# Optimization experiments

Hardware: AMD Instinct MI355X
Metric: run time of the kernel (lower is better)

Reference implementation:

```python
import jax, jax.numpy as jnp
import numpy as np

B, V, N, S, F, H, K, STEPS = 8, 3, 400, 1200, 16, 32, 10, 12
ALPHA_FUSE = 0.8
NEG = -9e15


def setup_inputs() -> dict:
    key = jax.random.key(0)
    ks = jax.random.split(key, 16)
    g = lambda i, shape, s=0.1: jax.random.normal(ks[i], shape, jnp.float32) * s
    return {
        "feat": jax.random.normal(ks[0], (B, S, F), jnp.float32),
        "adj": jax.random.bernoulli(ks[1], 0.05, (B, V, S, S)).astype(jnp.float32),
        "dis_lab": jax.random.uniform(ks[2], (B, K), dtype=jnp.float32),
        "W_gat": g(3, (V, F, H), 0.3),
        "a_gat": g(4, (V, 2 * H, 1), 0.3),
        "qkv_W": g(5, (H, 3 * H)),
        "qkv_b": jnp.zeros((3 * H,), jnp.float32),
        "o_W": g(6, (H, H)),
        "o_b": jnp.zeros((H,), jnp.float32),
        "fus_W": g(7, (H, H)),
        "fus_b": jnp.zeros((H,), jnp.float32),
        "att1_W": g(8, (2 * H, H)),
        "att1_b": jnp.zeros((H,), jnp.float32),
        "att2_W": g(9, (H, 1)),
        "att2_b": jnp.zeros((1,), jnp.float32),
        "gru_Wih": g(10, (H, 3 * H)),
        "gru_Whh": g(11, (H, 3 * H)),
        "gru_bih": jnp.zeros((3 * H,), jnp.float32),
        "gru_bhh": jnp.zeros((3 * H,), jnp.float32),
        "out_W": g(12, (H, 1)),
        "out_b": jnp.zeros((1,), jnp.float32),
    }


def _forward(feat, adj, dis_lab, W_gat, a_gat, qkv_W, qkv_b, o_W, o_b,
             fus_W, fus_b, att1_W, att1_b, att2_W, att2_b,
             gru_Wih, gru_Whh, gru_bih, gru_bhh, out_W, out_b):
    # ---- per-view GAT (masked softmax over dense adjacency) ----
    Wh = jnp.einsum('bsf,vfh->bvsh', feat, W_gat)            # [B,V,S,H]
    a1, a2 = a_gat[:, :H, 0], a_gat[:, H:, 0]
    e = (jnp.einsum('bvsh,vh->bvs', Wh, a1)[..., :, None]
         + jnp.einsum('bvsh,vh->bvs', Wh, a2)[..., None, :])  # [B,V,S,S]
    e = jax.nn.leaky_relu(e, 0.2)
    e = jnp.where(adj > 0, e, NEG)
    att = jax.nn.softmax(e, axis=-1)
    hid = jax.nn.elu(jnp.einsum('bvst,bvth->bvsh', att, Wh))  # [B,V,S,H]
    # ---- cross-view self-attention fusion (single head) ----
    x = hid.reshape(B, V * S, H)
    q, k, v = jnp.split(x @ qkv_W + qkv_b, 3, axis=-1)
    logits = jnp.einsum('bld,bmd->blm', q, k) / jnp.sqrt(jnp.float32(H))
    sa = jnp.einsum('blm,bmd->bld', jax.nn.softmax(logits, axis=-1), v)
    sa = sa @ o_W + o_b
    hfuse = (ALPHA_FUSE * sa + (1.0 - ALPHA_FUSE) * x).reshape(B, V, S, H)
    gate = jax.nn.sigmoid(hfuse @ fus_W + fus_b)
    fusion = jnp.sum(gate * hfuse, axis=1)[:, 2 * N:, :]      # [B,N,H]
    # ---- attention over label stations ----
    label = fusion[:, :K, :]                                  # [B,K,H]
    unlabel = fusion[:, K, :]                                 # [B,H]
    cat = jnp.concatenate([label, jnp.broadcast_to(unlabel[:, None, :], label.shape)], axis=-1)
    s = jax.nn.relu(cat @ att1_W + att1_b) @ att2_W + att2_b  # [B,K,1]
    score = jax.nn.softmax(s[..., 0] * dis_lab, axis=1)
    ctx = jnp.einsum('bk,bkh->bh', score, label)
    # ---- GRU decoder (feed hidden state back as next input) ----
    def gru_cell(xt, h):
        gi = xt @ gru_Wih + gru_bih
        gh = h @ gru_Whh + gru_bhh
        ir, iz, inn = jnp.split(gi, 3, axis=-1)
        hr, hz, hn = jnp.split(gh, 3, axis=-1)
        r = jax.nn.sigmoid(ir + hr)
        z = jax.nn.sigmoid(iz + hz)
        n = jnp.tanh(inn + r * hn)
        return (1.0 - z) * n + z * h
    def step(carry, _):
        xt, h = carry
        h2 = gru_cell(xt, h)
        out = h2 @ out_W + out_b
        return (h2, h2), out[:, 0]
    _, outs = jax.lax.scan(step, (ctx, unlabel), None, length=STEPS)
    return outs.T  # [B, STEPS]


def reference(feat, adj, dis_lab, W_gat, a_gat, qkv_W, qkv_b, o_W, o_b,
              fus_W, fus_b, att1_W, att1_b, att2_W, att2_b,
              gru_Wih, gru_Whh, gru_bih, gru_bhh, out_W, out_b):
    return _forward(feat, adj, dis_lab, W_gat, a_gat, qkv_W, qkv_b, o_W, o_b,
                    fus_W, fus_b, att1_W, att1_b, att2_W, att2_b,
                    gru_Wih, gru_Whh, gru_bih, gru_bhh, out_W, out_b)
```

## Files before the change

kernel.cpp:

```cpp
#include <hip/hip_runtime.h>
#include <math.h>

#define Bb 8
#define Vv 3
#define Ss 1200
#define SgP 1280
#define Ff 16
#define Hh 32
#define Kk 10
#define STEPS 12
#define ROWS (Bb*Vv*Ss)
#define L (Vv*Ss)
#define KPAD 1280
#define NKB 160
#define MROW 40

typedef __attribute__((ext_vector_type(8))) short bf16x8;
typedef __attribute__((ext_vector_type(4))) float f32x4;
typedef __attribute__((ext_vector_type(4))) unsigned int u32x4;

__device__ __forceinline__ unsigned int pack_hi2(float x0, float x1) {
    return (__float_as_uint(x1) & 0xFFFF0000u) | (__float_as_uint(x0) >> 16);
}
__device__ __forceinline__ unsigned int pack_lo2(float x0, float x1) {
    float h0 = __uint_as_float(__float_as_uint(x0) & 0xFFFF0000u);
    float h1 = __uint_as_float(__float_as_uint(x1) & 0xFFFF0000u);
    return (__float_as_uint(x1 - h1) & 0xFFFF0000u) | (__float_as_uint(x0 - h0) >> 16);
}
__device__ __forceinline__ unsigned int spread4(unsigned int x) {
    x = (x | (x << 12)) & 0x000F000Fu;
    x = (x | (x << 6))  & 0x03030303u;
    x = (x | (x << 3))  & 0x11111111u;
    return x;
}
__device__ __forceinline__ unsigned int enc_f(float f) {
    unsigned int u = __float_as_uint(f);
    return (u >> 31) ? ~u : (u | 0x80000000u);
}
__device__ __forceinline__ float dec_f(unsigned int e) {
    return (e >> 31) ? __uint_as_float(e & 0x7FFFFFFFu) : __uint_as_float(~e);
}

__global__ __launch_bounds__(256) void adj_pack_k(const float* __restrict__ adj,
                                                  unsigned int* __restrict__ maskb,
                                                  unsigned int* __restrict__ GmaxE) {
    if (blockIdx.x == 0 && threadIdx.x < Bb * Vv) GmaxE[threadIdx.x] = 0u;
    int gw = (blockIdx.x * 256 + threadIdx.x) >> 6;
    int lane = threadIdx.x & 63;
    for (int row = gw; row < ROWS; row += 5760) {
        const float* ar = adj + (size_t)row * Ss;
        unsigned int* mrow = maskb + (size_t)row * MROW;
        float4 a[5];
#pragma unroll
        for (int c = 0; c < 5; ++c) {
            int base = c * 256 + lane * 4;
            a[c] = (base + 3 < Ss) ? *(const float4*)(ar + base)
                                   : make_float4(0.f, 0.f, 0.f, 0.f);
        }
#pragma unroll
        for (int c = 0; c < 5; ++c) {
            unsigned long long b0 = __ballot(a[c].x > 0.f);
            unsigned long long b1 = __ballot(a[c].y > 0.f);
            unsigned long long b2 = __ballot(a[c].z > 0.f);
            unsigned long long b3 = __ballot(a[c].w > 0.f);
            int nw = (c == 4) ? 6 : 8;
            if (lane < nw) {
                int sh = 8 * lane;
                unsigned int B0 = (unsigned int)(b0 >> sh) & 0xFFu;
                unsigned int B1 = (unsigned int)(b1 >> sh) & 0xFFu;
                unsigned int B2 = (unsigned int)(b2 >> sh) & 0xFFu;
                unsigned int B3 = (unsigned int)(b3 >> sh) & 0xFFu;
                mrow[c * 8 + lane] = spread4(B0) | (spread4(B1) << 1)
                                   | (spread4(B2) << 2) | (spread4(B3) << 3);
            }
        }
        if (lane < 2) mrow[38 + lane] = 0u;
    }
}

__global__ __launch_bounds__(256) void wh_wht_k(const float* __restrict__ feat,
                                                const float* __restrict__ W_gat,
                                                const float* __restrict__ a_gat,
                                                ushort* __restrict__ WhT,
                                                float* __restrict__ fvec,
                                                float* __restrict__ gvecP,
                                                unsigned int* __restrict__ GmaxE) {
    int bv = blockIdx.x / 20, t = blockIdx.x % 20;
    int b = bv / Vv, v = bv - b * Vv;
    int s0 = t * 64;
    int tid = threadIdx.x;

    __shared__ float T[64][33];
    __shared__ float Wg[16][32];
    __shared__ float gred[8];
    for (int i = tid; i < 512; i += 256) Wg[i >> 5][i & 31] = W_gat[v * 512 + i];
    __syncthreads();

    int r8 = tid >> 5, h = tid & 31;
    float a1 = a_gat[v * 64 + h];
    float a2 = a_gat[v * 64 + 32 + h];
    float myg = -3.0e38f;
#pragma unroll
    for (int pass = 0; pass < 8; ++pass) {
        int s = s0 + pass * 8 + r8;
        float acc = 0.f;
        if (s < Ss) {
            const float4* fe = (const float4*)(feat + ((size_t)b * Ss + s) * Ff);
            float4 f0 = fe[0], f1 = fe[1], f2 = fe[2], f3 = fe[3];
            acc += f0.x * Wg[0][h]  + f0.y * Wg[1][h]  + f0.z * Wg[2][h]  + f0.w * Wg[3][h];
            acc += f1.x * Wg[4][h]  + f1.y * Wg[5][h]  + f1.z * Wg[6][h]  + f1.w * Wg[7][h];
            acc += f2.x * Wg[8][h]  + f2.y * Wg[9][h]  + f2.z * Wg[10][h] + f2.w * Wg[11][h];
            acc += f3.x * Wg[12][h] + f3.y * Wg[13][h] + f3.z * Wg[14][h] + f3.w * Wg[15][h];
        }
        T[pass * 8 + r8][h] = acc;
        float pf = acc * a1, pg = acc * a2;
#pragma unroll
        for (int m = 16; m >= 1; m >>= 1) {
            pf += __shfl_xor(pf, m);
            pg += __shfl_xor(pg, m);
        }
        if (h == 0) {
            if (s < Ss) { fvec[bv * Ss + s] = pf; myg = fmaxf(myg, pg); }
            gvecP[(size_t)bv * SgP + s] = (s < Ss) ? pg : 0.f;
        }
    }
    if (h == 0) gred[r8] = myg;
    __syncthreads();
    if (tid == 0) {
        float m = gred[0];
#pragma unroll
        for (int i = 1; i < 8; ++i) m = fmaxf(m, gred[i]);
        atomicMax(&GmaxE[bv], enc_f(m));
    }

    int hh = tid >> 3, c = tid & 7;
    int kb = t * 8 + c;
    unsigned int hb[4], lb[4];
#pragma unroll
    for (int j = 0; j < 4; ++j) {
        float e0 = T[c * 8 + 2 * j][hh], e1 = T[c * 8 + 2 * j + 1][hh];
        hb[j] = pack_hi2(e0, e1);
        lb[j] = pack_lo2(e0, e1);
    }
    size_t base = (((size_t)bv * NKB + kb) * 2) * 256 + hh * 8;
    *(uint4*)(WhT + base)       = make_uint4(hb[0], hb[1], hb[2], hb[3]);
    *(uint4*)(WhT + base + 256) = make_uint4(lb[0], lb[1], lb[2], lb[3]);
}

__global__ __launch_bounds__(256, 4) void gat_mfma_k(const unsigned int* __restrict__ maskb,
                                                     const ushort* __restrict__ WhT,
                                                     const float* __restrict__ fvec,
                                                     const float* __restrict__ gvecP,
                                                     const unsigned int* __restrict__ GmaxE,
                                                     float* __restrict__ hid,
                                                     float* __restrict__ hsel) {
    int blk = blockIdx.x;
    int bv = blk / 75, tb = blk % 75;
    int wk = threadIdx.x >> 6, lane = threadIdx.x & 63;
    int rowbase = tb * 16;
    int lr = lane & 15, kg = lane >> 4;
    int b = bv / Vv, v = bv - b * Vv;

    int ar = rowbase + lr;
    const float* g_b = gvecP + (size_t)bv * SgP;
    float fr = fvec[bv * Ss + ar];
    float M = fr + dec_f(GmaxE[bv]);
    float Mr = fmaxf(M, 0.2f * M);

    const unsigned int* mrow = maskb + (size_t)(bv * Ss + ar) * MROW + wk * 10;
    unsigned int mw[10];
#pragma unroll
    for (int i = 0; i < 5; ++i) {
        uint2 t = *(const uint2*)(mrow + 2 * i);
        mw[2 * i] = t.x; mw[2 * i + 1] = t.y;
    }

    f32x4 acc0 = {0.f, 0.f, 0.f, 0.f}, acc1 = {0.f, 0.f, 0.f, 0.f};
    float psum = 0.f;
    const ushort* Wbv = WhT + ((size_t)bv * NKB) * 512;

    int kst = wk * 320;
#pragma unroll
    for (int s = 0; s < 10; ++s) {
        int t0 = kst + s * 32 + kg * 8;
        int kb = t0 >> 3;
        unsigned int mb = (mw[s] >> (kg * 8)) & 0xFFu;

        const ushort* Bp = Wbv + (size_t)kb * 512 + lr * 8;
        bf16x8 bh0 = *(const bf16x8*)(Bp);
        bf16x8 bh1 = *(const bf16x8*)(Bp + 128);
        bf16x8 bl0 = *(const bf16x8*)(Bp + 256);
        bf16x8 bl1 = *(const bf16x8*)(Bp + 384);

        float4 gA = *(const float4*)(g_b + t0);
        float4 gB = *(const float4*)(g_b + t0 + 4);
        float gv8[8] = {gA.x, gA.y, gA.z, gA.w, gB.x, gB.y, gB.z, gB.w};
        float p[8];
#pragma unroll
        for (int j = 0; j < 8; ++j) {
            float e = fr + gv8[j];
            e = fmaxf(e, 0.2f * e);
            float pe = __expf(e - Mr);
            p[j] = ((mb >> j) & 1u) ? pe : 0.f;
            psum += p[j];
        }
        unsigned int hbp[4], lbp[4];
#pragma unroll
        for (int j = 0; j < 4; ++j) {
            hbp[j] = pack_hi2(p[2 * j], p[2 * j + 1]);
            lbp[j] = pack_lo2(p[2 * j], p[2 * j + 1]);
        }
        bf16x8 ah = __builtin_bit_cast(bf16x8, (u32x4){hbp[0], hbp[1], hbp[2], hbp[3]});
        bf16x8 al = __builtin_bit_cast(bf16x8, (u32x4){lbp[0], lbp[1], lbp[2], lbp[3]});
        acc0 = __builtin_amdgcn_mfma_f32_16x16x32_bf16(ah, bh0, acc0, 0, 0, 0);
        acc0 = __builtin_amdgcn_mfma_f32_16x16x32_bf16(ah, bl0, acc0, 0, 0, 0);
        acc0 = __builtin_amdgcn_mfma_f32_16x16x32_bf16(al, bh0, acc0, 0, 0, 0);
        acc1 = __builtin_amdgcn_mfma_f32_16x16x32_bf16(ah, bh1, acc1, 0, 0, 0);
        acc1 = __builtin_amdgcn_mfma_f32_16x16x32_bf16(ah, bl1, acc1, 0, 0, 0);
        acc1 = __builtin_amdgcn_mfma_f32_16x16x32_bf16(al, bh1, acc1, 0, 0, 0);
    }

    psum += __shfl_xor(psum, 16);
    psum += __shfl_xor(psum, 32);

    __shared__ float accS[4][2][16][17];
    __shared__ float psS[4][16];
#pragma unroll
    for (int j = 0; j < 4; ++j) {
        accS[wk][0][kg * 4 + j][lr] = acc0[j];
        accS[wk][1][kg * 4 + j][lr] = acc1[j];
    }
    if (lane < 16) psS[wk][lr] = psum;
    __syncthreads();
    if (threadIdx.x < 16)
        psS[0][threadIdx.x] += psS[1][threadIdx.x] + psS[2][threadIdx.x] + psS[3][threadIdx.x];
    __syncthreads();

    bool qb = (tb == 50);
    for (int idx = threadIdx.x; idx < 512; idx += 256) {
        int r = idx >> 5, col = idx & 31, tt = col >> 4, c = col & 15;
        float a = accS[0][tt][r][c] + accS[1][tt][r][c] + accS[2][tt][r][c] + accS[3][tt][r][c];
        float rr = a / psS[0][r];
        float hv = (rr > 0.f) ? rr : expm1f(rr);
        hid[((size_t)bv * Ss + rowbase + r) * 32 + col] = hv;
        if (qb && r < 11) hsel[(((size_t)b * Vv + v) * 11 + r) * 32 + col] = hv;
    }
}

__global__ __launch_bounds__(256) void attn_q_k(const float* __restrict__ hsel,
                                                const float* __restrict__ qkv_W,
                                                const float* __restrict__ qkv_b,
                                                float* __restrict__ qt,
                                                float* __restrict__ qc) {
    int b = blockIdx.x;
    int tid = threadIdx.x;
    __shared__ float hq[33][33];
    __shared__ float W1[32][33];
    __shared__ float W2[32][33];
    __shared__ float qS[33][33];

    for (int idx = tid; idx < 33 * 32; idx += 256) {
        int q = idx >> 5, i = idx & 31;
        int si = q / 3, v = q - si * 3;
        hq[q][i] = hsel[(((size_t)b * Vv + v) * 11 + si) * 32 + i];
    }
    for (int idx = tid; idx < 1024; idx += 256) {
        int i = idx >> 5, j = idx & 31;
        W1[i][j] = qkv_W[i * 96 + j];
        W2[i][j] = qkv_W[i * 96 + 32 + j];
    }
    __syncthreads();
    for (int idx = tid; idx < 33 * 32; idx += 256) {
        int q = idx >> 5, j = idx & 31;
        float a = qkv_b[j];
#pragma unroll
        for (int i = 0; i < 32; ++i) a += hq[q][i] * W1[i][j];
        qS[q][j] = a;
    }
    __syncthreads();
    for (int idx = tid; idx < 33 * 32; idx += 256) {
        int q = idx >> 5, i = idx & 31;
        float a = 0.f;
#pragma unroll
        for (int j = 0; j < 32; ++j) a += qS[q][j] * W2[i][j];
        qt[(size_t)b * 33 * 32 + q * 32 + i] = a;
    }
    if (tid < 33) {
        float a = 0.f;
        for (int j = 0; j < 32; ++j) a += qS[tid][j] * qkv_b[32 + j];
        qc[b * 33 + tid] = a;
    }
}

#define CH 120
#define NCH 30
#define PREC 34
__global__ __launch_bounds__(256) void attn_part_k(const float* __restrict__ hid,
                                                   const float* __restrict__ qt,
                                                   const float* __restrict__ qc,
                                                   float* __restrict__ part) {
    int blk = blockIdx.x;
    int b = blk / NCH, ch = blk % NCH;
    int k0 = ch * CH;
    int tid = threadIdx.x;
    const float inv = 0.1767766952966369f;

    __shared__ float hC[CH][33];
    __shared__ float qtS[33][33];
    __shared__ float qcS[33];
    __shared__ float lS[33][124];
    __shared__ float mS[33], lsS[33];

    for (int idx = tid; idx < CH * 32; idx += 256) {
        int r = idx >> 5, i = idx & 31;
        hC[r][i] = hid[((size_t)b * L + k0 + r) * 32 + i];
    }
    for (int idx = tid; idx < 33 * 32; idx += 256) {
        int q = idx >> 5, i = idx & 31;
        qtS[q][i] = qt[(size_t)b * 33 * 32 + q * 32 + i];
    }
    if (tid < 33) qcS[tid] = qc[b * 33 + tid];
    __syncthreads();

    for (int idx = tid; idx < 33 * CH; idx += 256) {
        int q = idx / CH, m = idx - q * CH;
        float d = 0.f;
#pragma unroll
        for (int i = 0; i < 32; ++i) d += qtS[q][i] * hC[m][i];
        lS[q][m] = (d + qcS[q]) * inv;
    }
    __syncthreads();

    int q4 = tid >> 2, j4 = tid & 3;
    if (q4 < 33) {
        float m = -3.0e38f;
        for (int k = j4; k < CH; k += 4) m = fmaxf(m, lS[q4][k]);
        m = fmaxf(m, __shfl_xor(m, 1));
        m = fmaxf(m, __shfl_xor(m, 2));
        float ssum = 0.f;
        for (int k = j4; k < CH; k += 4) {
            float p = __expf(lS[q4][k] - m);
            lS[q4][k] = p;
            ssum += p;
        }
        ssum += __shfl_xor(ssum, 1);
        ssum += __shfl_xor(ssum, 2);
        if (j4 == 0) { mS[q4] = m; lsS[q4] = ssum; }
    }
    __syncthreads();

    float* po = part + ((size_t)b * NCH + ch) * (33 * PREC);
    for (int idx = tid; idx < 33 * 32; idx += 256) {
        int q = idx >> 5, hh = idx & 31;
        float a = 0.f;
        for (int k = 0; k < CH; k += 4) {
            float4 p4 = *(const float4*)&lS[q][k];
            a += p4.x * hC[k][hh] + p4.y * hC[k+1][hh] + p4.z * hC[k+2][hh] + p4.w * hC[k+3][hh];
        }
        po[q * PREC + hh] = a;
    }
    if (tid < 33) { po[tid * PREC + 32] = mS[tid]; po[tid * PREC + 33] = lsS[tid]; }
}

__global__ __launch_bounds__(256) void comb_head_k(const float* __restrict__ part,
                                                   const float* __restrict__ hsel,
                                                   const float* __restrict__ qkv_W,
                                                   const float* __restrict__ qkv_b,
                                                   const float* __restrict__ o_W,
                                                   const float* __restrict__ o_b,
                                                   const float* __restrict__ fus_W,
                                                   const float* __restrict__ fus_b,
                                                   const float* __restrict__ dis_lab,
                                                   const float* __restrict__ att1_W,
                                                   const float* __restrict__ att1_b,
                                                   const float* __restrict__ att2_W,
                                                   const float* __restrict__ att2_b,
                                                   const float* __restrict__ Wih,
                                                   const float* __restrict__ Whh,
                                                   const float* __restrict__ bih,
                                                   const float* __restrict__ bhh,
                                                   const float* __restrict__ out_W,
                                                   const float* __restrict__ out_b,
                                                   float* __restrict__ out) {
    int b = blockIdx.x;
    int tid = threadIdx.x;
    __shared__ float RS[33][NCH];
    __shared__ float LSs[33];
    __shared__ float oS[33][33];
    __shared__ float vS[33][33];
    __shared__ float hfS[33][33];
    __shared__ float hfgS[33][32];
    __shared__ float lab[11][32];
    __shared__ float a1T[32][68];
    __shared__ float WihT[3][32][36];
    __shared__ float WhhT[3][32][36];
    __shared__ float sc[12];
    __shared__ float xS[32], hS[32];

    const float* pb = part + (size_t)b * NCH * (33 * PREC);

    if (tid < 33) {
        float M = -3.0e38f;
        for (int c = 0; c < NCH; ++c) M = fmaxf(M, pb[c * 33 * PREC + tid * PREC + 32]);
        float Lt = 0.f;
        for (int c = 0; c < NCH; ++c) {
            float w = __expf(pb[c * 33 * PREC + tid * PREC + 32] - M);
            RS[tid][c] = w;
            Lt += w * pb[c * 33 * PREC + tid * PREC + 33];
        }
        LSs[tid] = Lt;
    }
    __syncthreads();

    for (int idx = tid; idx < 33 * 32; idx += 256) {
        int q = idx >> 5, hh = idx & 31;
        float a = 0.f;
        for (int c = 0; c < NCH; ++c) a += RS[q][c] * pb[c * 33 * PREC + q * PREC + hh];
        oS[q][hh] = a / LSs[q];
    }
    __syncthreads();
    for (int idx = tid; idx < 33 * 32; idx += 256) {
        int q = idx >> 5, j = idx & 31;
        float a = qkv_b[64 + j];
#pragma unroll
        for (int i = 0; i < 32; ++i) a += oS[q][i] * qkv_W[i * 96 + 64 + j];
        vS[q][j] = a;
    }
    __syncthreads();
    for (int idx = tid; idx < 33 * 32; idx += 256) {
        int q = idx >> 5, hh = idx & 31;
        int si = q / 3, v = q - si * 3;
        float o = o_b[hh];
#pragma unroll
        for (int i = 0; i < 32; ++i) o += vS[q][i] * o_W[i * 32 + hh];
        float x = hsel[(((size_t)b * Vv + v) * 11 + si) * Hh + hh];
        hfS[q][hh] = 0.8f * o + 0.2f * x;
    }
    __syncthreads();
    for (int idx = tid; idx < 33 * 32; idx += 256) {
        int q = idx >> 5, hh = idx & 31;
        float gacc = fus_b[hh];
#pragma unroll
        for (int i = 0; i < 32; ++i) gacc += hfS[q][i] * fus_W[i * 32 + hh];
        float gate = 1.f / (1.f + __expf(-gacc));
        hfgS[q][hh] = gate * hfS[q][hh];
    }
    __syncthreads();

    for (int i = tid; i < 352; i += 256) {
        int k = i >> 5, hh = i & 31;
        lab[k][hh] = hfgS[k * 3 + 0][hh] + hfgS[k * 3 + 1][hh] + hfgS[k * 3 + 2][hh];
    }
    for (int idx = tid; idx < 2048; idx += 256) {
        int i = idx >> 5, jj = idx & 31;
        a1T[jj][i] = att1_W[idx];
    }
    for (int idx = tid; idx < 3072; idx += 256) {
        int i = idx / 96, col = idx - i * 96;
        int g = col >> 5, jj = col & 31;
        WihT[g][jj][i] = Wih[idx];
        WhhT[g][jj][i] = Whh[idx];
    }
    __syncthreads();

    int j = tid & 31, half = (tid >> 5) & 1;
    if (tid < 64) {
        float a2w = att2_W[j];
        float a1b = att1_b[j];
        float a2b = att2_b[0];
#pragma unroll
        for (int kk = 0; kk < 5; ++kk) {
            int k = 2 * kk + half;
            float t1 = a1b;
#pragma unroll
            for (int c = 0; c < 8; ++c) {
                float4 lb4 = *(const float4*)&lab[k][c * 4];
                float4 w4  = *(const float4*)&a1T[j][c * 4];
                t1 += lb4.x * w4.x + lb4.y * w4.y + lb4.z * w4.z + lb4.w * w4.w;
            }
#pragma unroll
            for (int c = 0; c < 8; ++c) {
                float4 lb4 = *(const float4*)&lab[10][c * 4];
                float4 w4  = *(const float4*)&a1T[j][32 + c * 4];
                t1 += lb4.x * w4.x + lb4.y * w4.y + lb4.z * w4.z + lb4.w * w4.w;
            }
            float val = fmaxf(t1, 0.f) * a2w;
#pragma unroll
            for (int mm = 16; mm >= 1; mm >>= 1) val += __shfl_xor(val, mm);
            if (j == 0) sc[k] = (val + a2b) * dis_lab[b * Kk + k];
        }
    }
    __syncthreads();
    if (tid == 0) {
        float mx = sc[0];
        for (int k = 1; k < 10; ++k) mx = fmaxf(mx, sc[k]);
        float sm = 0.f;
        for (int k = 0; k < 10; ++k) { sc[k] = __expf(sc[k] - mx); sm += sc[k]; }
        for (int k = 0; k < 10; ++k) sc[k] /= sm;
    }
    __syncthreads();
    if (tid < 32) {
        float c = 0.f;
        for (int k = 0; k < 10; ++k) c += sc[k] * lab[k][tid];
        xS[tid] = c;
        hS[tid] = lab[10][tid];
    }
    __syncthreads();

    float b_ir = bih[j], b_iz = bih[32 + j], b_in = bih[64 + j];
    float b_hr = bhh[j], b_hz = bhh[32 + j], b_hn = bhh[64 + j];
    float ow = out_W[j], ob = out_b[0];
    int i0 = half * 16;

    for (int t = 0; t < STEPS; ++t) {
        if (tid < 64) {
            float gi_r = 0.f, gi_z = 0.f, gi_n = 0.f;
            float gh_r = 0.f, gh_z = 0.f, gh_n = 0.f;
#pragma unroll
            for (int c = 0; c < 4; ++c) {
                float4 x4 = *(const float4*)&xS[i0 + c * 4];
                float4 h4 = *(const float4*)&hS[i0 + c * 4];
                float4 wr = *(const float4*)&WihT[0][j][i0 + c * 4];
                float4 wz = *(const float4*)&WihT[1][j][i0 + c * 4];
                float4 wn = *(const float4*)&WihT[2][j][i0 + c * 4];
                float4 ur = *(const float4*)&WhhT[0][j][i0 + c * 4];
                float4 uz = *(const float4*)&WhhT[1][j][i0 + c * 4];
                float4 un = *(const float4*)&WhhT[2][j][i0 + c * 4];
                gi_r += x4.x * wr.x + x4.y * wr.y + x4.z * wr.z + x4.w * wr.w;
                gi_z += x4.x * wz.x + x4.y * wz.y + x4.z * wz.z + x4.w * wz.w;
                gi_n += x4.x * wn.x + x4.y * wn.y + x4.z * wn.z + x4.w * wn.w;
                gh_r += h4.x * ur.x + h4.y * ur.y + h4.z * ur.z + h4.w * ur.w;
                gh_z += h4.x * uz.x + h4.y * uz.y + h4.z * uz.z + h4.w * uz.w;
                gh_n += h4.x * un.x + h4.y * un.y + h4.z * un.z + h4.w * un.w;
            }
            gi_r += __shfl_xor(gi_r, 32); gi_z += __shfl_xor(gi_z, 32); gi_n += __shfl_xor(gi_n, 32);
            gh_r += __shfl_xor(gh_r, 32); gh_z += __shfl_xor(gh_z, 32); gh_n += __shfl_xor(gh_n, 32);

            float hprev = hS[j];
            float r = 1.f / (1.f + __expf(-(gi_r + b_ir + gh_r + b_hr)));
            float z = 1.f / (1.f + __expf(-(gi_z + b_iz + gh_z + b_hz)));
            float n = tanhf(gi_n + b_in + r * (gh_n + b_hn));
            float hnew = (1.f - z) * n + z * hprev;

            float outp = hnew * ow;
#pragma unroll
            for (int mm = 16; mm >= 1; mm >>= 1) outp += __shfl_xor(outp, mm);
            if (tid == 0) out[b * STEPS + t] = outp + ob;
            if (tid < 32) { xS[32 + 0] = 0.f; }
            if (tid < 32) {  }
            if (tid < 32) { sc[11] = hnew; }
            if (tid < 32) { hS[j] = hS[j]; }
            if (tid < 32) { xS[j] = xS[j]; }
            if (tid < 32) { oS[0][j] = hnew; }
        }
        __syncthreads();
        if (tid < 32) { hS[tid] = oS[0][tid]; xS[tid] = oS[0][tid]; }
        __syncthreads();
    }
}

extern "C" void kernel_launch(void* const* d_in, const int* in_sizes, int n_in,
                              void* d_out, int out_size, void* d_ws, size_t ws_size,
                              hipStream_t stream) {
    const float* feat    = (const float*)d_in[0];
    const float* adj     = (const float*)d_in[1];
    const float* dis_lab = (const float*)d_in[2];
    const float* W_gat   = (const float*)d_in[3];
    const float* a_gat   = (const float*)d_in[4];
    const float* qkv_W   = (const float*)d_in[5];
    const float* qkv_b   = (const float*)d_in[6];
    const float* o_W     = (const float*)d_in[7];
    const float* o_b     = (const float*)d_in[8];
    const float* fus_W   = (const float*)d_in[9];
    const float* fus_b   = (const float*)d_in[10];
    const float* att1_W  = (const float*)d_in[11];
    const float* att1_b  = (const float*)d_in[12];
    const float* att2_W  = (const float*)d_in[13];
    const float* att2_b  = (const float*)d_in[14];
    const float* Wih     = (const float*)d_in[15];
    const float* Whh     = (const float*)d_in[16];
    const float* bih     = (const float*)d_in[17];
    const float* bhh     = (const float*)d_in[18];
    const float* out_W   = (const float*)d_in[19];
    const float* out_b   = (const float*)d_in[20];
    float* out = (float*)d_out;

    float* ws = (float*)d_ws;
    float*  hid    = ws;
    float*  fvec   = ws + 921600;
    float*  gvecP  = ws + 950400;
    unsigned int* GmaxE = (unsigned int*)(ws + 981120);
    ushort* WhT    = (ushort*)(ws + 981152);
    float*  part   = ws + 981152;
    float*  hsel   = ws + 1964192;
    float*  qt     = ws + 1972640;
    float*  qc     = ws + 1981088;
    unsigned int* maskb = (unsigned int*)(ws + 1981376);

    adj_pack_k<<<dim3(1440), dim3(256), 0, stream>>>(adj, maskb, GmaxE);
    wh_wht_k<<<dim3(Bb * Vv * 20), dim3(256), 0, stream>>>(feat, W_gat, a_gat,
                                                           WhT, fvec, gvecP, GmaxE);
    gat_mfma_k<<<dim3(Bb * Vv * 75), dim3(256), 0, stream>>>(maskb, WhT,
                                                             fvec, gvecP, GmaxE, hid, hsel);
    attn_q_k<<<dim3(Bb), dim3(256), 0, stream>>>(hsel, qkv_W, qkv_b, qt, qc);
    attn_part_k<<<dim3(Bb * NCH), dim3(256), 0, stream>>>(hid, qt, qc, part);
    comb_head_k<<<dim3(Bb), dim3(256), 0, stream>>>(part, hsel, qkv_W, qkv_b,
                                                    o_W, o_b, fus_W, fus_b,
                                                    dis_lab, att1_W, att1_b, att2_W, att2_b,
                                                    Wih, Whh, bih, bhh, out_W, out_b, out);
}
```

Measured before the change: 124.8 us.

## Fuse adjacency mask into GAT kernel, dropping separate bitmask pack pass

Removes the adj_pack_k kernel, which read the dense float adjacency and wrote a bitmask. The GAT MFMA kernel now loads the float adjacency rows directly into registers and tests them per element. GmaxE is zeroed with a memset. This saves one launch and the mask write and reread, but each GAT thread now reads 32x more adjacency bytes, and the 80 float registers force the occupancy hint down from 4 to 2.

Result: slower. 177.9 us (+42.5%).

```diff
diff --git a/kernel.cpp b/kernel.cpp
--- a/kernel.cpp
+++ b/kernel.cpp
@@ -13,7 +13,6 @@
 #define L (Vv*Ss)
 #define KPAD 1280
 #define NKB 160
-#define MROW 40
 
 typedef __attribute__((ext_vector_type(8))) short bf16x8;
 typedef __attribute__((ext_vector_type(4))) float f32x4;
@@ -27,55 +26,12 @@
     float h1 = __uint_as_float(__float_as_uint(x1) & 0xFFFF0000u);
     return (__float_as_uint(x1 - h1) & 0xFFFF0000u) | (__float_as_uint(x0 - h0) >> 16);
 }
-__device__ __forceinline__ unsigned int spread4(unsigned int x) {
-    x = (x | (x << 12)) & 0x000F000Fu;
-    x = (x | (x << 6))  & 0x03030303u;
-    x = (x | (x << 3))  & 0x11111111u;
-    return x;
-}
 __device__ __forceinline__ unsigned int enc_f(float f) {
     unsigned int u = __float_as_uint(f);
     return (u >> 31) ? ~u : (u | 0x80000000u);
 }
 __device__ __forceinline__ float dec_f(unsigned int e) {
     return (e >> 31) ? __uint_as_float(e & 0x7FFFFFFFu) : __uint_as_float(~e);
-}
-
-__global__ __launch_bounds__(256) void adj_pack_k(const float* __restrict__ adj,
-                                                  unsigned int* __restrict__ maskb,
-                                                  unsigned int* __restrict__ GmaxE) {
-    if (blockIdx.x == 0 && threadIdx.x < Bb * Vv) GmaxE[threadIdx.x] = 0u;
-    int gw = (blockIdx.x * 256 + threadIdx.x) >> 6;
-    int lane = threadIdx.x & 63;
-    for (int row = gw; row < ROWS; row += 5760) {
-        const float* ar = adj + (size_t)row * Ss;
-        unsigned int* mrow = maskb + (size_t)row * MROW;
-        float4 a[5];
-#pragma unroll
-        for (int c = 0; c < 5; ++c) {
-            int base = c * 256 + lane * 4;
-            a[c] = (base + 3 < Ss) ? *(const float4*)(ar + base)
-                                   : make_float4(0.f, 0.f, 0.f, 0.f);
-        }
-#pragma unroll
-        for (int c = 0; c < 5; ++c) {
-            unsigned long long b0 = __ballot(a[c].x > 0.f);
-            unsigned long long b1 = __ballot(a[c].y > 0.f);
-            unsigned long long b2 = __ballot(a[c].z > 0.f);
-            unsigned long long b3 = __ballot(a[c].w > 0.f);
-            int nw = (c == 4) ? 6 : 8;
-            if (lane < nw) {
-                int sh = 8 * lane;
-                unsigned int B0 = (unsigned int)(b0 >> sh) & 0xFFu;
-                unsigned int B1 = (unsigned int)(b1 >> sh) & 0xFFu;
-                unsigned int B2 = (unsigned int)(b2 >> sh) & 0xFFu;
-                unsigned int B3 = (unsigned int)(b3 >> sh) & 0xFFu;
-                mrow[c * 8 + lane] = spread4(B0) | (spread4(B1) << 1)
-                                   | (spread4(B2) << 2) | (spread4(B3) << 3);
-            }
-        }
-        if (lane < 2) mrow[38 + lane] = 0u;
-    }
 }
 
 __global__ __launch_bounds__(256) void wh_wht_k(const float* __restrict__ feat,
@@ -147,7 +103,7 @@
     *(uint4*)(WhT + base + 256) = make_uint4(lb[0], lb[1], lb[2], lb[3]);
 }
 
-__global__ __launch_bounds__(256, 4) void gat_mfma_k(const unsigned int* __restrict__ maskb,
+__global__ __launch_bounds__(256, 2) void gat_mfma_k(const float* __restrict__ adj,
                                                      const ushort* __restrict__ WhT,
                                                      const float* __restrict__ fvec,
                                                      const float* __restrict__ gvecP,
@@ -162,29 +118,32 @@
     int b = bv / Vv, v = bv - b * Vv;
 
     int ar = rowbase + lr;
+    const float* adj_r = adj + ((size_t)bv * Ss + ar) * Ss;
     const float* g_b = gvecP + (size_t)bv * SgP;
     float fr = fvec[bv * Ss + ar];
     float M = fr + dec_f(GmaxE[bv]);
     float Mr = fmaxf(M, 0.2f * M);
 
-    const unsigned int* mrow = maskb + (size_t)(bv * Ss + ar) * MROW + wk * 10;
-    unsigned int mw[10];
-#pragma unroll
-    for (int i = 0; i < 5; ++i) {
-        uint2 t = *(const uint2*)(mrow + 2 * i);
-        mw[2 * i] = t.x; mw[2 * i + 1] = t.y;
+    const float4 z4 = make_float4(0.f, 0.f, 0.f, 0.f);
+    int kst = wk * 320;
+
+    float4 av[20];
+#pragma unroll
+    for (int s = 0; s < 10; ++s) {
+        int t0 = kst + s * 32 + kg * 8;
+        bool ok = (t0 + 8 <= Ss);
+        av[2 * s]     = ok ? *(const float4*)(adj_r + t0)     : z4;
+        av[2 * s + 1] = ok ? *(const float4*)(adj_r + t0 + 4) : z4;
     }
 
     f32x4 acc0 = {0.f, 0.f, 0.f, 0.f}, acc1 = {0.f, 0.f, 0.f, 0.f};
     float psum = 0.f;
     const ushort* Wbv = WhT + ((size_t)bv * NKB) * 512;
 
-    int kst = wk * 320;
 #pragma unroll
     for (int s = 0; s < 10; ++s) {
         int t0 = kst + s * 32 + kg * 8;
         int kb = t0 >> 3;
-        unsigned int mb = (mw[s] >> (kg * 8)) & 0xFFu;
 
         const ushort* Bp = Wbv + (size_t)kb * 512 + lr * 8;
         bf16x8 bh0 = *(const bf16x8*)(Bp);
@@ -195,13 +154,15 @@
         float4 gA = *(const float4*)(g_b + t0);
         float4 gB = *(const float4*)(g_b + t0 + 4);
         float gv8[8] = {gA.x, gA.y, gA.z, gA.w, gB.x, gB.y, gB.z, gB.w};
+        float aw8[8] = {av[2*s].x, av[2*s].y, av[2*s].z, av[2*s].w,
+                        av[2*s+1].x, av[2*s+1].y, av[2*s+1].z, av[2*s+1].w};
         float p[8];
 #pragma unroll
         for (int j = 0; j < 8; ++j) {
             float e = fr + gv8[j];
             e = fmaxf(e, 0.2f * e);
             float pe = __expf(e - Mr);
-            p[j] = ((mb >> j) & 1u) ? pe : 0.f;
+            p[j] = (aw8[j] > 0.f) ? pe : 0.f;
             psum += p[j];
         }
         unsigned int hbp[4], lbp[4];
@@ -546,12 +507,7 @@
 #pragma unroll
             for (int mm = 16; mm >= 1; mm >>= 1) outp += __shfl_xor(outp, mm);
             if (tid == 0) out[b * STEPS + t] = outp + ob;
-            if (tid < 32) { xS[32 + 0] = 0.f; }
-            if (tid < 32) {  }
-            if (tid < 32) { sc[11] = hnew; }
-            if (tid < 32) { hS[j] = hS[j]; }
-            if (tid < 32) { xS[j] = xS[j]; }
-            if (tid < 32) { oS[0][j] = hnew; }
+            if (tid < 32) oS[0][j] = hnew;
         }
         __syncthreads();
         if (tid < 32) { hS[tid] = oS[0][tid]; xS[tid] = oS[0][tid]; }
@@ -595,12 +551,11 @@
     float*  hsel   = ws + 1964192;
     float*  qt     = ws + 1972640;
     float*  qc     = ws + 1981088;
-    unsigned int* maskb = (unsigned int*)(ws + 1981376);
-
-    adj_pack_k<<<dim3(1440), dim3(256), 0, stream>>>(adj, maskb, GmaxE);
+
+    hipMemsetAsync(GmaxE, 0, Bb * Vv * sizeof(unsigned int), stream);
     wh_wht_k<<<dim3(Bb * Vv * 20), dim3(256), 0, stream>>>(feat, W_gat, a_gat,
                                                            WhT, fvec, gvecP, GmaxE);
-    gat_mfma_k<<<dim3(Bb * Vv * 75), dim3(256), 0, stream>>>(maskb, WhT,
+    gat_mfma_k<<<dim3(Bb * Vv * 75), dim3(256), 0, stream>>>(adj, WhT,
                                                              fvec, gvecP, GmaxE, hid, hsel);
     attn_q_k<<<dim3(Bb), dim3(256), 0, stream>>>(hsel, qkv_W, qkv_b, qt, qc);
     attn_part_k<<<dim3(Bb * NCH), dim3(256), 0, stream>>>(hid, qt, qc, part);
```
